# Kernel tuning notes

Measured on AMD Instinct MI355X. Metric: run time of the kernel, lower is better.

Reference implementation:

```python
import jax, jax.numpy as jnp
import numpy as np

HEADS = 4
HEAD_DIM = 128  # GATConv out_channels
NEG_SLOPE_ATT = 0.2   # GATConv internal leaky relu
NEG_SLOPE_ACT = 0.01  # nn.LeakyReLU() default


def gat_conv(x, edge_index, W, att_src, att_dst, bias):
    # x: [N, F]; edge_index: [2, E] (row 0 = src j, row 1 = dst i)
    N = x.shape[0]
    h = (x @ W).reshape(N, HEADS, HEAD_DIM)            # [N, H, C]
    loops = jnp.arange(N, dtype=edge_index.dtype)
    src = jnp.concatenate([edge_index[0], loops])      # add self loops
    dst = jnp.concatenate([edge_index[1], loops])
    a_src = jnp.einsum('nhc,hc->nh', h, att_src)       # [N, H]
    a_dst = jnp.einsum('nhc,hc->nh', h, att_dst)
    e = jax.nn.leaky_relu(a_src[src] + a_dst[dst], NEG_SLOPE_ATT)  # [E', H]
    # segment softmax over incoming edges of each dst node
    emax = jax.ops.segment_max(e, dst, num_segments=N)
    ex = jnp.exp(e - emax[dst])
    denom = jax.ops.segment_sum(ex, dst, num_segments=N)
    alpha = ex / (denom[dst] + 1e-16)                  # [E', H]
    msg = h[src] * alpha[:, :, None]                   # [E', H, C]
    out = jax.ops.segment_sum(msg, dst, num_segments=N)
    return out.reshape(N, HEADS * HEAD_DIM) + bias     # [N, H*C]


def branch(x, edge_index, W, att_src, att_dst, bias, fc1_w, fc1_b):
    h = gat_conv(x, edge_index, W, att_src, att_dst, bias)
    h = jax.nn.leaky_relu(h, NEG_SLOPE_ACT)
    g = jnp.mean(h, axis=0, keepdims=True)             # global mean pool, batch all zeros -> [1, H*C]
    g = jax.nn.leaky_relu(g @ fc1_w + fc1_b, NEG_SLOPE_ACT)
    return g  # dropout is identity in eval mode


def setup_inputs() -> dict:
    key = jax.random.key(0)
    ks = jax.random.split(key, 10)
    N, E, F = 20000, 320000, 512
    HC = HEADS * HEAD_DIM
    s = 1.0 / np.sqrt(F)
    return {
        'x': jax.random.normal(ks[0], (N, F), jnp.float32),
        'adj': jax.random.randint(ks[1], (2, E), 0, N, jnp.int64),
        'wt_x': jax.random.normal(ks[2], (N, F), jnp.float32),
        'wt_adj': jax.random.randint(ks[3], (2, E), 0, N, jnp.int64),
        'W': jax.random.normal(ks[4], (F, HC), jnp.float32) * s,
        'att_src': jax.random.normal(ks[5], (HEADS, HEAD_DIM), jnp.float32) * s,
        'att_dst': jax.random.normal(ks[6], (HEADS, HEAD_DIM), jnp.float32) * s,
        'bias': jnp.zeros((HC,), jnp.float32),
        'fc1_w': jax.random.normal(ks[7], (HC, 512), jnp.float32) * (1.0 / np.sqrt(HC)),
        'fc1_b': jnp.zeros((512,), jnp.float32),
    }


def reference(x, adj, wt_x, wt_adj, W, att_src, att_dst, bias, fc1_w, fc1_b):
    g = branch(x, adj, W, att_src, att_dst, bias, fc1_w, fc1_b)
    wt_g = branch(wt_x, wt_adj, W, att_src, att_dst, bias, fc1_w, fc1_b)
    xd = g - wt_g
    return jnp.concatenate([g, wt_g, xd], axis=1)  # [1, 3*512]
```

## Files before the change

### kernel.cpp

```cpp
#include <hip/hip_runtime.h>
#include <hip/hip_bf16.h>

typedef unsigned short u16;
typedef short bf16x8 __attribute__((ext_vector_type(8)));
typedef float f32x4 __attribute__((ext_vector_type(4)));
typedef float f32x2 __attribute__((ext_vector_type(2)));

__device__ __forceinline__ u16 f2b(float f) {
    unsigned x = __float_as_uint(f);
    return (u16)((x + 0x7fffu + ((x >> 16) & 1u)) >> 16);
}

__device__ __forceinline__ int pkbf(float lo, float hi) {
    return __builtin_amdgcn_perm(__float_as_uint(hi), __float_as_uint(lo), 0x07060302);
}

__device__ __forceinline__ void pkfma(f32x2& acc, f32x2 f, f32x2 ex) {
    asm("v_pk_fma_f32 %0, %1, %2, %0" : "+v"(acc) : "v"(f), "v"(ex));
}

__global__ void cast_wt_kernel(const float* __restrict__ W, u16* __restrict__ Wt) {
    int idx = blockIdx.x * blockDim.x + threadIdx.x;
    int n = idx >> 9, k = idx & 511;
    Wt[idx] = f2b(W[k * 512 + n]);
}

__global__ __launch_bounds__(256, 2) void gemm_fused2(
    const float* __restrict__ xA, const float* __restrict__ xW, const u16* __restrict__ Bt,
    unsigned char* __restrict__ h8, const float* __restrict__ att_src,
    const float* __restrict__ att_dst, float* __restrict__ asrc, float* __restrict__ adst,
    int N, int Mpad) {
    __shared__ float lA[128 * 32];
    __shared__ u16 lB[128 * 32];
    __shared__ float sred[2][128][2];
    const int tid = threadIdx.x;
    const int w = tid >> 6, l = tid & 63;
    const int row0 = blockIdx.y * 128;
    const int head = blockIdx.x;
    const int col0 = head * 128;
    const int wr = w >> 1, wc = w & 1;
    const int mlane = l & 15, quad = l >> 4;
    const int R2v = 2 * Mpad;

    const float* src = (row0 >= Mpad) ? xW : xA;
    const int rbase = row0 - (row0 >= Mpad ? Mpad : 0);
    const int arow = (w << 3) + (l >> 3);
    const int acol = (l & 7) << 2;
    const int srow = (w << 4) + (l >> 2);
    const int scol = (l & 3) << 3;

    f32x4 acc[4][4];
#pragma unroll
    for (int i = 0; i < 4; i++)
#pragma unroll
        for (int j = 0; j < 4; j++) acc[i][j] = f32x4{0.f, 0.f, 0.f, 0.f};

    for (int k0 = 0; k0 < 512; k0 += 32) {
#pragma unroll
        for (int g = 0; g < 4; ++g) {
            int lrow = rbase + g * 32 + arow;
            lrow = min(lrow, N - 1);
            const float* ga = src + (size_t)lrow * 512 + k0 + acol;
            float* la = lA + (g * 32 + (w << 3)) * 32;
            __builtin_amdgcn_global_load_lds((const __attribute__((address_space(1))) void*)ga,
                                             (__attribute__((address_space(3))) void*)la, 16, 0, 0);
        }
#pragma unroll
        for (int s = 0; s < 2; ++s) {
            const u16* gb = Bt + (size_t)(col0 + s * 64 + srow) * 512 + (k0 + scol);
            u16* lb = lB + s * 2048 + w * 512;
            __builtin_amdgcn_global_load_lds((const __attribute__((address_space(1))) void*)gb,
                                             (__attribute__((address_space(3))) void*)lb, 16, 0, 0);
        }
        __syncthreads();
        bf16x8 af[4], bfr[4];
#pragma unroll
        for (int i = 0; i < 4; i++) {
            const float* ap = &lA[(wr * 64 + i * 16 + mlane) * 32 + quad * 8];
            float4 f0 = *(const float4*)ap;
            float4 f1 = *(const float4*)(ap + 4);
            int* ai = (int*)&af[i];
            ai[0] = pkbf(f0.x, f0.y);
            ai[1] = pkbf(f0.z, f0.w);
            ai[2] = pkbf(f1.x, f1.y);
            ai[3] = pkbf(f1.z, f1.w);
            bfr[i] = *(const bf16x8*)&lB[(wc * 64 + i * 16 + mlane) * 32 + quad * 8];
        }
#pragma unroll
        for (int i = 0; i < 4; i++)
#pragma unroll
            for (int j = 0; j < 4; j++)
                acc[i][j] = __builtin_amdgcn_mfma_f32_16x16x32_bf16(af[i], bfr[j], acc[i][j], 0, 0, 0);
        __syncthreads();
    }

    float as_j[4], ad_j[4];
#pragma unroll
    for (int j = 0; j < 4; j++) {
        as_j[j] = att_src[col0 + wc * 64 + j * 16 + mlane];
        ad_j[j] = att_dst[col0 + wc * 64 + j * 16 + mlane];
    }
#pragma unroll
    for (int i = 0; i < 4; i++) {
#pragma unroll
        for (int r = 0; r < 4; r++) {
            float vs = 0.f, vd = 0.f;
#pragma unroll
            for (int j = 0; j < 4; j++) {
                float hv = acc[i][j][r];
                vs += hv * as_j[j];
                vd += hv * ad_j[j];
            }
#pragma unroll
            for (int o = 8; o >= 1; o >>= 1) {
                vs += __shfl_xor(vs, o);
                vd += __shfl_xor(vd, o);
            }
            if (mlane == 0) {
                int lrow = wr * 64 + i * 16 + quad * 4 + r;
                sred[0][lrow][wc] = vs;
                sred[1][lrow][wc] = vd;
            }
        }
    }
#pragma unroll
    for (int i = 0; i < 4; i++)
#pragma unroll
        for (int j = 0; j < 4; j++)
#pragma unroll
            for (int r = 0; r < 4; r++) {
                int rg = row0 + wr * 64 + i * 16 + quad * 4 + r;
                int cc = wc * 64 + j * 16 + mlane;
                float v = acc[i][j][r];
                unsigned pk = __builtin_amdgcn_cvt_pk_fp8_f32(v, v, 0, false);
                h8[(((size_t)(head * R2v + rg)) << 7) + cc] = (unsigned char)(pk & 0xff);
            }
    __syncthreads();
    {
        int row = tid & 127, which = tid >> 7;
        int rg = row0 + row;
        float v = sred[which][row][0] + sred[which][row][1];
        (which ? adst : asrc)[head * R2v + rg] = v;
    }
}

__global__ void csr_count(const int* __restrict__ adj, const int* __restrict__ wadj,
                          int E, int Mpad, int* __restrict__ deg) {
    int i = blockIdx.x * blockDim.x + threadIdx.x;
    if (i < 2 * E) {
        int d = (i < E) ? adj[E + i] : (wadj[E + (i - E)] + Mpad);
        atomicAdd(&deg[d], 1);
    }
}

__global__ __launch_bounds__(256) void scanA(const int* __restrict__ deg, int* __restrict__ off,
                                             int* __restrict__ bsum, int n, int N, int Mpad) {
    __shared__ int wsum[4];
    int tid = threadIdx.x, lane = tid & 63, wid = tid >> 6;
    int i = blockIdx.x * 256 + tid;
    int valid = (i < N) || (i >= Mpad && i < Mpad + N);
    int d = (i < n) ? deg[i] + (valid ? 1 : 0) : 0;
    int x = d;
#pragma unroll
    for (int o = 1; o < 64; o <<= 1) {
        int y = __shfl_up(x, (unsigned)o, 64);
        if (lane >= o) x += y;
    }
    if (lane == 63) wsum[wid] = x;
    __syncthreads();
    int woff = 0;
    for (int j = 0; j < wid; ++j) woff += wsum[j];
    if (i < n) off[i] = woff + x - d;
    if (tid == 255) bsum[blockIdx.x] = woff + x;
}

__global__ __launch_bounds__(256) void scanB(const int* __restrict__ bsum, int* __restrict__ bbase,
                                             int nb, int* __restrict__ off, int n) {
    __shared__ int wsum[4];
    int tid = threadIdx.x, lane = tid & 63, wid = tid >> 6;
    int d = (tid < nb) ? bsum[tid] : 0;
    int x = d;
#pragma unroll
    for (int o = 1; o < 64; o <<= 1) {
        int y = __shfl_up(x, (unsigned)o, 64);
        if (lane >= o) x += y;
    }
    if (lane == 63) wsum[wid] = x;
    __syncthreads();
    int woff = 0;
    for (int j = 0; j < wid; ++j) woff += wsum[j];
    int excl = woff + x - d;
    if (tid < nb) bbase[tid] = excl;
    if (tid == nb - 1) off[n] = excl + d;
}

__global__ void scanC(int* __restrict__ off, const int* __restrict__ bbase,
                      int* __restrict__ cursor, int* __restrict__ csrc, int n, int N, int Mpad) {
    int i = blockIdx.x * blockDim.x + threadIdx.x;
    if (i < n) {
        int o = off[i] + bbase[i >> 8];
        off[i] = o;
        int valid = (i < N) || (i >= Mpad && i < Mpad + N);
        if (valid) csrc[o] = i;
        cursor[i] = o + valid;
    }
}

__global__ void csr_scatter(const int* __restrict__ adj, const int* __restrict__ wadj,
                            int E, int Mpad, int* __restrict__ cursor, int* __restrict__ csrc) {
    int i = blockIdx.x * blockDim.x + threadIdx.x;
    if (i < 2 * E) {
        int s, d;
        if (i < E) {
            s = adj[i];
            d = adj[E + i];
        } else {
            s = wadj[i - E] + Mpad;
            d = wadj[E + (i - E)] + Mpad;
        }
        int p = atomicAdd(&cursor[d], 1);
        csrc[p] = s;
    }
}

__global__ __launch_bounds__(256, 4) void gat_aggregate11(
    const unsigned char* __restrict__ h8, const float* __restrict__ asrc,
    const float* __restrict__ adst, const int* __restrict__ off, const int* __restrict__ csrc,
    const float* __restrict__ bias, float* __restrict__ partAB, int Mpad) {
    const int R2 = 2 * Mpad;
    __shared__ float spool[128];
    int tid = threadIdx.x;
    if (tid < 128) spool[tid] = 0.f;
    __syncthreads();
    const int wv = tid >> 6, l = tid & 63;
    const int gi = (l >> 3) & 3;
    const int hi = l >> 5;
    const int chb = (l & 7) << 4;
    const int head = (blockIdx.x & 7) >> 1;
    const int gc = blockIdx.x & 1;
    const unsigned char* h8h = h8 + (((size_t)head * R2) << 7);
    const float* ash = asrc + (size_t)head * R2;
    const float* adh = adst + (size_t)head * R2;
    float bb[16];
#pragma unroll
    for (int k = 0; k < 16; ++k) bb[k] = bias[head * 128 + chb + k];
    float pool[16];
#pragma unroll
    for (int k = 0; k < 16; ++k) pool[k] = 0.f;

    const int hb = gc * Mpad;
    const int half = Mpad >> 1;
    int widx = ((blockIdx.x >> 3) << 2) + wv;

    for (int p = widx; p < half; p += 1024) {
        int d0 = (p << 1) + hb;
        int q0 = off[d0], q1 = off[d0 + 1], q2 = off[d0 + 2];
        int n0 = q1 - q0, n1 = q2 - q1;
        int nmax = max(n0, n1);
        if (nmax == 0) continue;
        int nm = hi ? n1 : n0;
        int qm = hi ? q1 : q0;
        float ad = adh[d0 + hi];
        f32x2 acc2[8];
#pragma unroll
        for (int j = 0; j < 8; ++j) acc2[j] = f32x2{0.f, 0.f};
        float dsum = 0.f;

        int i0 = gi, i1 = 4 + gi, i2 = 8 + gi, i3 = 12 + gi;
        int E0 = csrc[qm + ((i0 < nm) ? i0 : 0)];
        int E1 = csrc[qm + ((i1 < nm) ? i1 : 0)];
        int E2 = csrc[qm + ((i2 < nm) ? i2 : 0)];
        int E3 = csrc[qm + ((i3 < nm) ? i3 : 0)];
        float A0 = ash[E0];
        int4 H0 = *(const int4*)(h8h + (((size_t)E0) << 7) + chb);
        float A1 = ash[E1];
        int4 H1 = *(const int4*)(h8h + (((size_t)E1) << 7) + chb);

        for (int base = 0; base < nmax; base += 4) {
            int i4 = base + 16 + gi;
            int E4 = csrc[qm + ((i4 < nm) ? i4 : 0)];
            float A2 = ash[E2];
            int4 H2 = *(const int4*)(h8h + (((size_t)E2) << 7) + chb);
            float e = A0 + ad;
            float em = fmaxf(e, 0.2f * e);
            float ex = __expf(em);
            ex = ((base + gi) < nm) ? ex : 0.f;
            dsum += ex;
            f32x2 exv = {ex, ex};
            f32x2 f;
            f = __builtin_amdgcn_cvt_pk_f32_fp8(H0.x, false); pkfma(acc2[0], f, exv);
            f = __builtin_amdgcn_cvt_pk_f32_fp8(H0.x, true);  pkfma(acc2[1], f, exv);
            f = __builtin_amdgcn_cvt_pk_f32_fp8(H0.y, false); pkfma(acc2[2], f, exv);
            f = __builtin_amdgcn_cvt_pk_f32_fp8(H0.y, true);  pkfma(acc2[3], f, exv);
            f = __builtin_amdgcn_cvt_pk_f32_fp8(H0.z, false); pkfma(acc2[4], f, exv);
            f = __builtin_amdgcn_cvt_pk_f32_fp8(H0.z, true);  pkfma(acc2[5], f, exv);
            f = __builtin_amdgcn_cvt_pk_f32_fp8(H0.w, false); pkfma(acc2[6], f, exv);
            f = __builtin_amdgcn_cvt_pk_f32_fp8(H0.w, true);  pkfma(acc2[7], f, exv);
            A0 = A1; H0 = H1;
            A1 = A2; H1 = H2;
            E2 = E3; E3 = E4;
        }
        dsum += __shfl_xor(dsum, 8);
        dsum += __shfl_xor(dsum, 16);
#pragma unroll
        for (int j = 0; j < 8; ++j) {
            acc2[j].x += __shfl_xor(acc2[j].x, 8);
            acc2[j].y += __shfl_xor(acc2[j].y, 8);
            acc2[j].x += __shfl_xor(acc2[j].x, 16);
            acc2[j].y += __shfl_xor(acc2[j].y, 16);
        }
        if (nm > 0) {
            float inv = 1.f / (dsum + 1e-16f);
#pragma unroll
            for (int j = 0; j < 8; ++j) {
                float o0 = acc2[j].x * inv + bb[2 * j];
                float o1 = acc2[j].y * inv + bb[2 * j + 1];
                pool[2 * j] += fmaxf(o0, 0.01f * o0);
                pool[2 * j + 1] += fmaxf(o1, 0.01f * o1);
            }
        }
    }
    if ((l & 31) < 8) {
#pragma unroll
        for (int k = 0; k < 16; ++k) atomicAdd(&spool[chb + k], pool[k]);
    }
    __syncthreads();
    if (tid < 128) {
        int slot = (blockIdx.x >> 3) & 63;
        float* dp = partAB + (gc ? 64 * 512 : 0) + (slot << 9) + head * 128 + tid;
        atomicAdd(dp, spool[tid]);
    }
}

__global__ __launch_bounds__(256) void fc_final2(
    const float* __restrict__ partAB, const float* __restrict__ w, const float* __restrict__ b,
    float* __restrict__ out, float invN) {
    __shared__ float gA[512], gB[512];
    __shared__ float rA[256], rB[256];
    int t = threadIdx.x;
    for (int i = t; i < 512; i += 256) {
        float sA = 0.f, sB = 0.f;
        for (int r = 0; r < 64; ++r) {
            sA += partAB[r * 512 + i];
            sB += partAB[64 * 512 + r * 512 + i];
        }
        gA[i] = sA * invN;
        gB[i] = sB * invN;
    }
    __syncthreads();
    int jj = t & 31, ks = t >> 5;
    int j = blockIdx.x * 32 + jj;
    float sA = 0.f, sB = 0.f;
    for (int k = ks * 64; k < ks * 64 + 64; ++k) {
        float wv = w[k * 512 + j];
        sA += gA[k] * wv;
        sB += gB[k] * wv;
    }
    rA[t] = sA;
    rB[t] = sB;
    __syncthreads();
    if (ks == 0) {
#pragma unroll
        for (int s2 = 1; s2 < 8; ++s2) {
            sA += rA[jj + 32 * s2];
            sB += rB[jj + 32 * s2];
        }
        sA += b[j];
        sB += b[j];
        sA = sA >= 0.f ? sA : 0.01f * sA;
        sB = sB >= 0.f ? sB : 0.01f * sB;
        out[j] = sA;
        out[512 + j] = sB;
        out[1024 + j] = sA - sB;
    }
}

extern "C" void kernel_launch(void* const* d_in, const int* in_sizes, int n_in,
                              void* d_out, int out_size, void* d_ws, size_t ws_size,
                              hipStream_t stream) {
    const float* x = (const float*)d_in[0];
    const int* adj = (const int*)d_in[1];
    const float* wtx = (const float*)d_in[2];
    const int* wadj = (const int*)d_in[3];
    const float* W = (const float*)d_in[4];
    const float* att_s = (const float*)d_in[5];
    const float* att_d = (const float*)d_in[6];
    const float* bias = (const float*)d_in[7];
    const float* fc1w = (const float*)d_in[8];
    const float* fc1b = (const float*)d_in[9];
    float* out = (float*)d_out;

    const int N = in_sizes[0] / 512;
    const int E = in_sizes[1] / 2;
    const int Mpad = ((N + 127) / 128) * 128;
    const int R2 = 2 * Mpad;
    const int nb = (R2 + 255) / 256;

    char* p = (char*)d_ws;
    auto alloc = [&](size_t bytes) -> char* {
        char* r = p;
        p += (bytes + 255) & ~(size_t)255;
        return r;
    };
    unsigned char* h8 = (unsigned char*)alloc((size_t)R2 * 512);
    u16* Wt = (u16*)alloc(512 * 512 * 2);
    float* asrc = (float*)alloc((size_t)R2 * 4 * 4);
    float* adst = (float*)alloc((size_t)R2 * 4 * 4);
    int* deg = (int*)alloc((size_t)R2 * 4);
    int* off = (int*)alloc((size_t)(R2 + 1) * 4);
    int* cursor = (int*)alloc((size_t)R2 * 4);
    int* bsum = (int*)alloc(256 * 4);
    int* bbase = (int*)alloc(256 * 4);
    int* csrc = (int*)alloc((size_t)2 * (E + N) * 4);
    float* partAB = (float*)alloc((size_t)2 * 64 * 512 * 4);

    hipMemsetAsync(partAB, 0, (size_t)2 * 64 * 512 * 4, stream);
    hipMemsetAsync(deg, 0, (size_t)R2 * 4, stream);
    cast_wt_kernel<<<(512 * 512) / 256, 256, 0, stream>>>(W, Wt);

    csr_count<<<(2 * E + 255) / 256, 256, 0, stream>>>(adj, wadj, E, Mpad, deg);
    scanA<<<nb, 256, 0, stream>>>(deg, off, bsum, R2, N, Mpad);
    scanB<<<1, 256, 0, stream>>>(bsum, bbase, nb, off, R2);
    scanC<<<nb, 256, 0, stream>>>(off, bbase, cursor, csrc, R2, N, Mpad);
    csr_scatter<<<(2 * E + 255) / 256, 256, 0, stream>>>(adj, wadj, E, Mpad, cursor, csrc);

    dim3 gg(4, R2 / 128, 1);
    gemm_fused2<<<gg, 256, 0, stream>>>(x, wtx, Wt, h8, att_s, att_d, asrc, adst, N, Mpad);

    gat_aggregate11<<<2048, 256, 0, stream>>>(h8, asrc, adst, off, csrc, bias, partAB, Mpad);

    fc_final2<<<16, 256, 0, stream>>>(partAB, fc1w, fc1b, out, 1.0f / (float)N);
}
```

Measured before the change: 343.0 us.

## Load edge indices and attention scores once per lane group and broadcast via shuffles

Only the lead lane of each 8-lane group now loads the CSR source indices and source attention scores, then broadcasts them with wave shuffles. The other seven lanes, which read identical addresses, no longer issue redundant global loads. The grid also doubles to 4096 blocks with a matching wave stride, which adds parallelism and smaller per-wave work. The cost is extra shuffle instructions and divergent branches in the inner loop, which may lengthen its latency chain.

```diff
diff --git a/kernel.cpp b/kernel.cpp
--- a/kernel.cpp
+++ b/kernel.cpp
@@ -223,7 +223,7 @@
     }
 }
 
-__global__ __launch_bounds__(256, 4) void gat_aggregate11(
+__global__ __launch_bounds__(256, 4) void gat_aggregate12(
     const unsigned char* __restrict__ h8, const float* __restrict__ asrc,
     const float* __restrict__ adst, const int* __restrict__ off, const int* __restrict__ csrc,
     const float* __restrict__ bias, float* __restrict__ partAB, int Mpad) {
@@ -236,6 +236,8 @@
     const int gi = (l >> 3) & 3;
     const int hi = l >> 5;
     const int chb = (l & 7) << 4;
+    const bool lead = (l & 7) == 0;
+    const int lsrc = l & 56;
     const int head = (blockIdx.x & 7) >> 1;
     const int gc = blockIdx.x & 1;
     const unsigned char* h8h = h8 + (((size_t)head * R2) << 7);
@@ -252,7 +254,7 @@
     const int half = Mpad >> 1;
     int widx = ((blockIdx.x >> 3) << 2) + wv;
 
-    for (int p = widx; p < half; p += 1024) {
+    for (int p = widx; p < half; p += 2048) {
         int d0 = (p << 1) + hb;
         int q0 = off[d0], q1 = off[d0 + 1], q2 = off[d0 + 2];
         int n0 = q1 - q0, n1 = q2 - q1;
@@ -266,21 +268,37 @@
         for (int j = 0; j < 8; ++j) acc2[j] = f32x2{0.f, 0.f};
         float dsum = 0.f;
 
-        int i0 = gi, i1 = 4 + gi, i2 = 8 + gi, i3 = 12 + gi;
-        int E0 = csrc[qm + ((i0 < nm) ? i0 : 0)];
-        int E1 = csrc[qm + ((i1 < nm) ? i1 : 0)];
-        int E2 = csrc[qm + ((i2 < nm) ? i2 : 0)];
-        int E3 = csrc[qm + ((i3 < nm) ? i3 : 0)];
-        float A0 = ash[E0];
-        int4 H0 = *(const int4*)(h8h + (((size_t)E0) << 7) + chb);
-        float A1 = ash[E1];
-        int4 H1 = *(const int4*)(h8h + (((size_t)E1) << 7) + chb);
-
+        int E2L = 0, E3L = 0;
+        float A0L = 0.f, A1L = 0.f;
+        int4 H0, H1;
+        {
+            int Ea = 0, Eb = 0;
+            if (lead) {
+                Ea = csrc[qm + ((gi < nm) ? gi : 0)];
+                Eb = csrc[qm + ((4 + gi < nm) ? 4 + gi : 0)];
+                E2L = csrc[qm + ((8 + gi < nm) ? 8 + gi : 0)];
+                E3L = csrc[qm + ((12 + gi < nm) ? 12 + gi : 0)];
+                A0L = ash[Ea];
+                A1L = ash[Eb];
+            }
+            int E0 = __shfl(Ea, lsrc);
+            int E1 = __shfl(Eb, lsrc);
+            H0 = *(const int4*)(h8h + (((size_t)E0) << 7) + chb);
+            H1 = *(const int4*)(h8h + (((size_t)E1) << 7) + chb);
+        }
+
+#pragma unroll 2
         for (int base = 0; base < nmax; base += 4) {
-            int i4 = base + 16 + gi;
-            int E4 = csrc[qm + ((i4 < nm) ? i4 : 0)];
-            float A2 = ash[E2];
+            int E4L = 0;
+            float A2L = 0.f;
+            if (lead) {
+                int i4 = base + 16 + gi;
+                E4L = csrc[qm + ((i4 < nm) ? i4 : 0)];
+                A2L = ash[E2L];
+            }
+            int E2 = __shfl(E2L, lsrc);
             int4 H2 = *(const int4*)(h8h + (((size_t)E2) << 7) + chb);
+            float A0 = __shfl(A0L, lsrc);
             float e = A0 + ad;
             float em = fmaxf(e, 0.2f * e);
             float ex = __expf(em);
@@ -296,9 +314,9 @@
             f = __builtin_amdgcn_cvt_pk_f32_fp8(H0.z, true);  pkfma(acc2[5], f, exv);
             f = __builtin_amdgcn_cvt_pk_f32_fp8(H0.w, false); pkfma(acc2[6], f, exv);
             f = __builtin_amdgcn_cvt_pk_f32_fp8(H0.w, true);  pkfma(acc2[7], f, exv);
-            A0 = A1; H0 = H1;
-            A1 = A2; H1 = H2;
-            E2 = E3; E3 = E4;
+            A0L = A1L; A1L = A2L;
+            E2L = E3L; E3L = E4L;
+            H0 = H1; H1 = H2;
         }
         dsum += __shfl_xor(dsum, 8);
         dsum += __shfl_xor(dsum, 16);
@@ -427,7 +445,7 @@
     dim3 gg(4, R2 / 128, 1);
     gemm_fused2<<<gg, 256, 0, stream>>>(x, wtx, Wt, h8, att_s, att_d, asrc, adst, N, Mpad);
 
-    gat_aggregate11<<<2048, 256, 0, stream>>>(h8, asrc, adst, off, csrc, bias, partAB, Mpad);
+    gat_aggregate12<<<4096, 256, 0, stream>>>(h8, asrc, adst, off, csrc, bias, partAB, Mpad);
 
     fc_final2<<<16, 256, 0, stream>>>(partAB, fc1w, fc1b, out, 1.0f / (float)N);
 }
```

Measured after the change: 346.3 us. No clear change (+1.0%).

## Retile GEMM to 64-row blocks covering all four heads per block

Applied to the files above, without the earlier changes.

The fused GEMM now uses 64-row tiles with each of the four waves owning one full head (128 columns), instead of 128x128 tiles indexed by head. Each x row tile is therefore loaded from global memory once rather than once per head, which cuts the dominant fp32 A-matrix traffic. Because a wave now holds a whole head, the attention-score dot products finish inside the wave, removing the shared-memory cross-wave reduction and its barrier. The cost is 32 accumulator tiles per wave, which raises register pressure and may hurt occupancy. Each block also loads the full 512-column B slice every k-step, which increases B traffic and LDS use.

```diff
diff --git a/kernel.cpp b/kernel.cpp
--- a/kernel.cpp
+++ b/kernel.cpp
@@ -25,58 +25,55 @@
     Wt[idx] = f2b(W[k * 512 + n]);
 }
 
-__global__ __launch_bounds__(256, 2) void gemm_fused2(
+__global__ __launch_bounds__(256, 2) void gemm_fused3(
     const float* __restrict__ xA, const float* __restrict__ xW, const u16* __restrict__ Bt,
     unsigned char* __restrict__ h8, const float* __restrict__ att_src,
     const float* __restrict__ att_dst, float* __restrict__ asrc, float* __restrict__ adst,
     int N, int Mpad) {
-    __shared__ float lA[128 * 32];
-    __shared__ u16 lB[128 * 32];
-    __shared__ float sred[2][128][2];
+    __shared__ float lA[64 * 32];
+    __shared__ u16 lB[512 * 32];
     const int tid = threadIdx.x;
     const int w = tid >> 6, l = tid & 63;
-    const int row0 = blockIdx.y * 128;
-    const int head = blockIdx.x;
-    const int col0 = head * 128;
-    const int wr = w >> 1, wc = w & 1;
+    const int row0 = blockIdx.x * 64;
+    const int head = w;
     const int mlane = l & 15, quad = l >> 4;
     const int R2v = 2 * Mpad;
 
     const float* src = (row0 >= Mpad) ? xW : xA;
     const int rbase = row0 - (row0 >= Mpad ? Mpad : 0);
-    const int arow = (w << 3) + (l >> 3);
+    const int arow = (l >> 3);
     const int acol = (l & 7) << 2;
-    const int srow = (w << 4) + (l >> 2);
-    const int scol = (l & 3) << 3;
-
-    f32x4 acc[4][4];
+    const int brow = (l >> 2);
+    const int bcol = (l & 3) << 3;
+
+    f32x4 acc[4][8];
 #pragma unroll
     for (int i = 0; i < 4; i++)
 #pragma unroll
-        for (int j = 0; j < 4; j++) acc[i][j] = f32x4{0.f, 0.f, 0.f, 0.f};
+        for (int j = 0; j < 8; j++) acc[i][j] = f32x4{0.f, 0.f, 0.f, 0.f};
 
     for (int k0 = 0; k0 < 512; k0 += 32) {
 #pragma unroll
-        for (int g = 0; g < 4; ++g) {
-            int lrow = rbase + g * 32 + arow;
+        for (int g = 0; g < 2; ++g) {
+            int lrow = rbase + (w << 4) + (g << 3) + arow;
             lrow = min(lrow, N - 1);
             const float* ga = src + (size_t)lrow * 512 + k0 + acol;
-            float* la = lA + (g * 32 + (w << 3)) * 32;
+            float* la = lA + (((w << 4) + (g << 3)) << 5);
             __builtin_amdgcn_global_load_lds((const __attribute__((address_space(1))) void*)ga,
                                              (__attribute__((address_space(3))) void*)la, 16, 0, 0);
         }
 #pragma unroll
-        for (int s = 0; s < 2; ++s) {
-            const u16* gb = Bt + (size_t)(col0 + s * 64 + srow) * 512 + (k0 + scol);
-            u16* lb = lB + s * 2048 + w * 512;
+        for (int s = 0; s < 8; ++s) {
+            const u16* gb = Bt + (size_t)((w << 7) + (s << 4) + brow) * 512 + (k0 + bcol);
+            u16* lb = lB + (((w << 7) + (s << 4)) << 5);
             __builtin_amdgcn_global_load_lds((const __attribute__((address_space(1))) void*)gb,
                                              (__attribute__((address_space(3))) void*)lb, 16, 0, 0);
         }
         __syncthreads();
-        bf16x8 af[4], bfr[4];
+        bf16x8 af[4], bfr[8];
 #pragma unroll
         for (int i = 0; i < 4; i++) {
-            const float* ap = &lA[(wr * 64 + i * 16 + mlane) * 32 + quad * 8];
+            const float* ap = &lA[(i * 16 + mlane) * 32 + quad * 8];
             float4 f0 = *(const float4*)ap;
             float4 f1 = *(const float4*)(ap + 4);
             int* ai = (int*)&af[i];
@@ -84,21 +81,23 @@
             ai[1] = pkbf(f0.z, f0.w);
             ai[2] = pkbf(f1.x, f1.y);
             ai[3] = pkbf(f1.z, f1.w);
-            bfr[i] = *(const bf16x8*)&lB[(wc * 64 + i * 16 + mlane) * 32 + quad * 8];
-        }
+        }
+#pragma unroll
+        for (int j = 0; j < 8; j++)
+            bfr[j] = *(const bf16x8*)&lB[((w << 7) + j * 16 + mlane) * 32 + quad * 8];
 #pragma unroll
         for (int i = 0; i < 4; i++)
 #pragma unroll
-            for (int j = 0; j < 4; j++)
+            for (int j = 0; j < 8; j++)
                 acc[i][j] = __builtin_amdgcn_mfma_f32_16x16x32_bf16(af[i], bfr[j], acc[i][j], 0, 0, 0);
         __syncthreads();
     }
 
-    float as_j[4], ad_j[4];
-#pragma unroll
-    for (int j = 0; j < 4; j++) {
-        as_j[j] = att_src[col0 + wc * 64 + j * 16 + mlane];
-        ad_j[j] = att_dst[col0 + wc * 64 + j * 16 + mlane];
+    float as_j[8], ad_j[8];
+#pragma unroll
+    for (int j = 0; j < 8; j++) {
+        as_j[j] = att_src[(head << 7) + j * 16 + mlane];
+        ad_j[j] = att_dst[(head << 7) + j * 16 + mlane];
     }
 #pragma unroll
     for (int i = 0; i < 4; i++) {
@@ -106,7 +105,7 @@
         for (int r = 0; r < 4; r++) {
             float vs = 0.f, vd = 0.f;
 #pragma unroll
-            for (int j = 0; j < 4; j++) {
+            for (int j = 0; j < 8; j++) {
                 float hv = acc[i][j][r];
                 vs += hv * as_j[j];
                 vd += hv * ad_j[j];
@@ -117,31 +116,24 @@
                 vd += __shfl_xor(vd, o);
             }
             if (mlane == 0) {
-                int lrow = wr * 64 + i * 16 + quad * 4 + r;
-                sred[0][lrow][wc] = vs;
-                sred[1][lrow][wc] = vd;
+                int rg = row0 + i * 16 + quad * 4 + r;
+                asrc[head * R2v + rg] = vs;
+                adst[head * R2v + rg] = vd;
             }
         }
     }
 #pragma unroll
     for (int i = 0; i < 4; i++)
 #pragma unroll
-        for (int j = 0; j < 4; j++)
+        for (int j = 0; j < 8; j++)
 #pragma unroll
             for (int r = 0; r < 4; r++) {
-                int rg = row0 + wr * 64 + i * 16 + quad * 4 + r;
-                int cc = wc * 64 + j * 16 + mlane;
+                int rg = row0 + i * 16 + quad * 4 + r;
+                int cc = j * 16 + mlane;
                 float v = acc[i][j][r];
                 unsigned pk = __builtin_amdgcn_cvt_pk_fp8_f32(v, v, 0, false);
                 h8[(((size_t)(head * R2v + rg)) << 7) + cc] = (unsigned char)(pk & 0xff);
             }
-    __syncthreads();
-    {
-        int row = tid & 127, which = tid >> 7;
-        int rg = row0 + row;
-        float v = sred[which][row][0] + sred[which][row][1];
-        (which ? adst : asrc)[head * R2v + rg] = v;
-    }
 }
 
 __global__ void csr_count(const int* __restrict__ adj, const int* __restrict__ wadj,
@@ -424,8 +416,7 @@
     scanC<<<nb, 256, 0, stream>>>(off, bbase, cursor, csrc, R2, N, Mpad);
     csr_scatter<<<(2 * E + 255) / 256, 256, 0, stream>>>(adj, wadj, E, Mpad, cursor, csrc);
 
-    dim3 gg(4, R2 / 128, 1);
-    gemm_fused2<<<gg, 256, 0, stream>>>(x, wtx, Wt, h8, att_s, att_d, asrc, adst, N, Mpad);
+    gemm_fused3<<<R2 / 64, 256, 0, stream>>>(x, wtx, Wt, h8, att_s, att_d, asrc, adst, N, Mpad);
 
     gat_aggregate11<<<2048, 256, 0, stream>>>(h8, asrc, adst, off, csrc, bias, partAB, Mpad);
 
```

After: 342.3 us. No clear change (-0.2%).
